# Optimization experiments

Measured on AMD Instinct MI355X. Metric: run time of the kernel, lower is better.

The kernel has to match this reference:

```python
import jax, jax.numpy as jnp
import numpy as np

N, E, C = 100000, 50000, 256
M, D, F, T = 128, 128, 128, 64
MSG = 2 * D + F + T  # 448
T_MAX = 100000


def setup_inputs() -> dict:
    key = jax.random.key(0)
    ks = jax.random.split(key, 16)
    src = jax.random.randint(ks[0], (E,), 0, N, dtype=jnp.int32)
    dst = jax.random.randint(ks[1], (E,), 0, N, dtype=jnp.int32)
    t = jnp.sort(jax.random.randint(ks[2], (E,), 0, T_MAX, dtype=jnp.int32))
    last_update = jax.random.randint(ks[3], (N,), 0, 1000, dtype=jnp.int32)
    event_feat = jax.random.normal(ks[4], (E, F), dtype=jnp.float32)
    src_embeds = jax.random.normal(ks[5], (E, D), dtype=jnp.float32)
    dst_embeds = jax.random.normal(ks[6], (E, D), dtype=jnp.float32)
    nodes_memory = jax.random.normal(ks[7], (N, M), dtype=jnp.float32)
    incidence = jax.random.uniform(ks[8], (N, C), dtype=jnp.float32)
    w_time = jax.random.normal(ks[9], (T,), dtype=jnp.float32)
    b_time = jax.random.normal(ks[10], (T,), dtype=jnp.float32)
    W_ih = jax.random.normal(ks[11], (MSG, 3 * M), dtype=jnp.float32) * 0.05
    W_hh = jax.random.normal(ks[12], (M, 3 * M), dtype=jnp.float32) * 0.05
    b_ih = jnp.zeros((3 * M,), jnp.float32)
    b_hh = jnp.zeros((3 * M,), jnp.float32)
    return dict(src=src, dst=dst, t=t, last_update=last_update,
                event_feat=event_feat, src_embeds=src_embeds, dst_embeds=dst_embeds,
                nodes_memory=nodes_memory, incidence=incidence,
                w_time=w_time, b_time=b_time, W_ih=W_ih, W_hh=W_hh,
                b_ih=b_ih, b_hh=b_hh)


def reference(src, dst, t, last_update, event_feat, src_embeds, dst_embeds,
              nodes_memory, incidence, w_time, b_time, W_ih, W_hh, b_ih, b_hh):
    E2 = 2 * E
    # store_events: raw messages + flipped-direction messages, keyed by source node
    src_all = jnp.concatenate([src, dst])            # [2E]
    emb_s = jnp.concatenate([src_embeds, dst_embeds], axis=0)
    emb_d = jnp.concatenate([dst_embeds, src_embeds], axis=0)
    feat = jnp.concatenate([event_feat, event_feat], axis=0)
    t_all = jnp.concatenate([t, t])                  # [2E]
    # message function: concat(src_embed, dst_embed, event_feat, time_encoding(dt))
    dt = (t_all - last_update[src_all]).astype(jnp.float32)
    time_enc = jnp.cos(dt[:, None] * w_time[None, :] + b_time[None, :])  # [2E, T]
    msg = jnp.concatenate([emb_s, emb_d, feat, time_enc], axis=-1)       # [2E, MSG]
    # 'last' aggregation: per-node argmax over timestamps via rank-encoded segment_max
    perm = jnp.argsort(t_all)  # ascending time order
    rank = jnp.zeros((E2,), jnp.int32).at[perm].set(jnp.arange(E2, dtype=jnp.int32))
    seg_rank = jax.ops.segment_max(rank, src_all, num_segments=N)
    counts = jax.ops.segment_sum(jnp.ones((E2,), jnp.int32), src_all, num_segments=N)
    has_msg = counts > 0                              # [N]
    last_idx = perm[jnp.where(has_msg, seg_rank, 0)]  # [N] event index of last message
    agg_msg = msg[last_idx]                           # [N, MSG]
    # GRU memory updater (torch.nn.GRUCell convention)
    gx = agg_msg @ W_ih + b_ih
    gh = nodes_memory @ W_hh + b_hh
    xr, xz, xn = jnp.split(gx, 3, axis=-1)
    hr, hz, hn = jnp.split(gh, 3, axis=-1)
    r = jax.nn.sigmoid(xr + hr)
    z = jax.nn.sigmoid(xz + hz)
    n = jnp.tanh(xn + r * hn)
    h_new = (1.0 - z) * n + z * nodes_memory
    new_mem = jnp.where(has_msg[:, None], h_new, nodes_memory)  # [N, M]
    # rewire_graph: community memory = incidence.T @ nodes_memory
    comm_mem = jnp.einsum('nc,nm->cm', incidence, new_mem)      # [C, M]
    return jnp.concatenate([new_mem, comm_mem], axis=0)         # [N + C, M]
```

## Files before the change

kernel.cpp:

```cpp
#include <hip/hip_runtime.h>
#include <hip/hip_bf16.h>
#include <stdint.h>

#define N_NODES   100000
#define N_EVENTS  50000
#define N_COMM    256
#define DIM_M     128
#define K_TOT     576
#define GCOLS     512
#define INV2PI    0.15915494309189535f
#define XB_GRID   4096

typedef float f32x4 __attribute__((ext_vector_type(4)));
typedef short s16x8 __attribute__((ext_vector_type(8)));
typedef short s16x4 __attribute__((ext_vector_type(4)));

#define KEYS_OFF   0
#define CNT_OFF    800000
#define LIST_OFF   800008
#define WT_OFF     1200640
#define X_ROWS     100096
#define X_OFF      1790464
#define PART_M_OFF X_OFF
#define CT_NCH     256
#define CT_CPN     392
#define TMP2_OFF   (PART_M_OFF + 33554432)
#define TENC_OFF   1790464
#define PART_F_OFF 14594560

__device__ inline unsigned short f2bf(float x) {
    union { float f; unsigned u; } v; v.f = x;
    unsigned r = v.u + 0x7FFFu + ((v.u >> 16) & 1u);
    return (unsigned short)(r >> 16);
}
__device__ inline float bf2f(unsigned short u) {
    union { unsigned u; float f; } v; v.u = ((unsigned)u) << 16;
    return v.f;
}
__device__ inline float cos_rev(float rev) {
    float fr = rev - floorf(rev);
#if __has_builtin(__builtin_amdgcn_cosf)
    return __builtin_amdgcn_cosf(fr);
#else
    return cosf(fr * 6.283185307179586f);
#endif
}
__device__ inline float sigmoid_f(float x) { return 1.0f / (1.0f + __expf(-x)); }
__device__ inline float tanh_f(float x) {
    float t = __expf(2.0f * x);
    return 1.0f - 2.0f / (t + 1.0f);
}

__global__ __launch_bounds__(256) void k_agg(const int* __restrict__ src,
                                             const int* __restrict__ dst,
                                             const int* __restrict__ t,
                                             unsigned long long* __restrict__ keys) {
    int i = blockIdx.x * 256 + threadIdx.x;
    if (i >= 2 * N_EVENTS) return;
    int e = (i < N_EVENTS) ? i : i - N_EVENTS;
    int node = (i < N_EVENTS) ? src[i] : dst[e];
    unsigned long long key =
        ((unsigned long long)(unsigned)t[e] << 32) | (unsigned)(i + 1);
    atomicMax(&keys[node], key);
}

__global__ __launch_bounds__(256) void k_compact(const unsigned long long* __restrict__ keys,
                                                 unsigned int* __restrict__ cnt,
                                                 int* __restrict__ list) {
    int n = blockIdx.x * 256 + threadIdx.x;
    if (n >= N_NODES) return;
    if (keys[n] != 0ULL) {
        unsigned p = atomicAdd(cnt, 1u);
        list[p] = n;
    }
}

__global__ __launch_bounds__(256) void k_xbuild(
    const unsigned long long* __restrict__ keys,
    const unsigned int* __restrict__ cnt,
    const int* __restrict__ list,
    const int* __restrict__ t,
    const int* __restrict__ last_update,
    const float* __restrict__ event_feat,
    const float* __restrict__ src_embeds,
    const float* __restrict__ dst_embeds,
    const float* __restrict__ mem,
    const float* __restrict__ w_time,
    const float* __restrict__ b_time,
    const float* __restrict__ W_ih,
    const float* __restrict__ W_hh,
    unsigned short* __restrict__ Wt,
    unsigned short* __restrict__ X) {
    if (blockIdx.x >= XB_GRID) {
        int idx = (blockIdx.x - XB_GRID) * 256 + threadIdx.x;
        if (idx >= GCOLS * K_TOT) return;
        int col2 = idx / K_TOT, k = idx % K_TOT;
        int mh = col2 >> 8, rem = col2 & 255;
        int g = rem >> 6, m = mh * 64 + (rem & 63);
        float v;
        if (g == 0)      v = (k < 448) ? W_ih[(size_t)k * 384 + m]
                                       : W_hh[(size_t)(k - 448) * 384 + m];
        else if (g == 1) v = (k < 448) ? W_ih[(size_t)k * 384 + 128 + m]
                                       : W_hh[(size_t)(k - 448) * 384 + 128 + m];
        else if (g == 2) v = (k < 448) ? W_ih[(size_t)k * 384 + 256 + m] : 0.0f;
        else             v = (k < 448) ? 0.0f : W_hh[(size_t)(k - 448) * 384 + 256 + m];
        Wt[idx] = f2bf(v);
        return;
    }
    const unsigned c = *cnt;
    const unsigned cpad = (c + 127u) & ~127u;
    const unsigned total = cpad * 72u;
    for (unsigned idx = blockIdx.x * 256 + threadIdx.x; idx < total;
         idx += XB_GRID * 256) {
        const unsigned row = idx / 72u;
        const int s = (int)(idx - row * 72u);
        unsigned short* xp = X + (size_t)row * K_TOT + s * 8;
        s16x8 v;
        if (row >= c) {
#pragma unroll
            for (int j = 0; j < 8; ++j) v[j] = 0;
            *(s16x8*)xp = v;
            continue;
        }
        const int node = list[row];
        const unsigned long long key = keys[node];
        const int ia = (int)(key & 0xffffffffull) - 1;
        const int e = (ia < N_EVENTS) ? ia : ia - N_EVENTS;
        if (s < 48) {
            const float* p;
            if (s < 16)
                p = ((ia < N_EVENTS) ? src_embeds : dst_embeds) + (size_t)e * 128 + s * 8;
            else if (s < 32)
                p = ((ia < N_EVENTS) ? dst_embeds : src_embeds) + (size_t)e * 128 + (s - 16) * 8;
            else
                p = event_feat + (size_t)e * 128 + (s - 32) * 8;
            float4 a = *(const float4*)p;
            float4 b = *(const float4*)(p + 4);
            v[0] = (short)f2bf(a.x); v[1] = (short)f2bf(a.y);
            v[2] = (short)f2bf(a.z); v[3] = (short)f2bf(a.w);
            v[4] = (short)f2bf(b.x); v[5] = (short)f2bf(b.y);
            v[6] = (short)f2bf(b.z); v[7] = (short)f2bf(b.w);
        } else if (s < 56) {
            const float dt = (float)(t[e] - last_update[node]);
            const int c0 = (s - 48) * 8;
#pragma unroll
            for (int j = 0; j < 8; ++j) {
                float rev = fmaf(dt, w_time[c0 + j] * INV2PI, b_time[c0 + j] * INV2PI);
                v[j] = (short)f2bf(cos_rev(rev));
            }
        } else {
            const float* p = mem + (size_t)node * 128 + (s - 56) * 8;
            float4 a = *(const float4*)p;
            float4 b = *(const float4*)(p + 4);
            v[0] = (short)f2bf(a.x); v[1] = (short)f2bf(a.y);
            v[2] = (short)f2bf(a.z); v[3] = (short)f2bf(a.w);
            v[4] = (short)f2bf(b.x); v[5] = (short)f2bf(b.y);
            v[6] = (short)f2bf(b.z); v[7] = (short)f2bf(b.w);
        }
        *(s16x8*)xp = v;
    }
}

__global__ __launch_bounds__(512, 4) void k_gemm2(
    const unsigned int* __restrict__ cnt,
    const int* __restrict__ list,
    const unsigned short* __restrict__ X,
    const unsigned short* __restrict__ Wt,
    const float* __restrict__ b_ih,
    const float* __restrict__ b_hh,
    float* __restrict__ out) {
    __shared__ unsigned short As[3][128][32];
    __shared__ unsigned short Bs[3][256][32];
    __shared__ int Ls[128];

    const unsigned c = *cnt;
    const int rb = blockIdx.x >> 1;
    const int mh = blockIdx.x & 1;
    const int base = rb * 128;
    if ((unsigned)base >= c) return;
    const int tid = threadIdx.x;
    const int w = tid >> 6, l = tid & 63;
    const int lr = l & 15, lk = l >> 4;
    const int wm = w >> 2, wn = w & 3;

    if (tid < 128)
        Ls[tid] = ((unsigned)(base + tid) < c) ? list[base + tid] : 0;

    const int mcol = mh * 64 + wn * 16 + lr;

    unsigned short hreg[16];
#pragma unroll
    for (int rt = 0; rt < 4; ++rt)
#pragma unroll
        for (int reg = 0; reg < 4; ++reg) {
            const int r = wm * 64 + rt * 16 + lk * 4 + reg;
            hreg[rt * 4 + reg] = X[(size_t)(base + r) * K_TOT + 448 + mcol];
        }

    const int srow = tid >> 2;
    const int sd = tid & 3;
    const int ssl = (sd ^ ((srow >> 1) & 3)) << 3;
    const unsigned short* gA  = X  + (size_t)(base + srow) * K_TOT + ssl;
    const unsigned short* gB0 = Wt + (size_t)(mh * 256 + srow) * K_TOT + ssl;
    const unsigned short* gB1 = Wt + (size_t)(mh * 256 + 128 + srow) * K_TOT + ssl;

#define GLD(SRC, DST) __builtin_amdgcn_global_load_lds( \
        (const __attribute__((address_space(1))) unsigned int*)(SRC), \
        (__attribute__((address_space(3))) unsigned int*)(DST), 16, 0, 0)

    auto stage = [&](int ch, int buf) {
        GLD(gA  + ch * 32, &As[buf][w * 16][0]);
        GLD(gB0 + ch * 32, &Bs[buf][w * 16][0]);
        GLD(gB1 + ch * 32, &Bs[buf][128 + w * 16][0]);
    };

    f32x4 acc[4][4];
#pragma unroll
    for (int rt = 0; rt < 4; ++rt)
#pragma unroll
        for (int i = 0; i < 4; ++i) acc[rt][i] = (f32x4){0.f, 0.f, 0.f, 0.f};

    stage(0, 0);
    stage(1, 1);
    __syncthreads();

#pragma unroll
    for (int ch = 0; ch < 18; ++ch) {
        const int buf = ch % 3;
        if (ch <= 15) stage(ch + 2, (ch + 2) % 3);
        __builtin_amdgcn_s_setprio(1);
        s16x8 a[4];
#pragma unroll
        for (int rt = 0; rt < 4; ++rt) {
            const int r = wm * 64 + rt * 16 + lr;
            const int sl = lk ^ ((r >> 1) & 3);
            a[rt] = *(const s16x8*)&As[buf][r][sl << 3];
        }
#pragma unroll
        for (int i = 0; i < 4; ++i) {
            const int cl = i * 64 + wn * 16 + lr;
            const int slb = lk ^ ((cl >> 1) & 3);
            s16x8 b = *(const s16x8*)&Bs[buf][cl][slb << 3];
#pragma unroll
            for (int rt = 0; rt < 4; ++rt)
                acc[rt][i] = __builtin_amdgcn_mfma_f32_16x16x32_bf16(
                    a[rt], b, acc[rt][i], 0, 0, 0);
        }
        __builtin_amdgcn_s_setprio(0);
        if (ch < 17) {
            __builtin_amdgcn_sched_barrier(0);
            if (ch < 16) asm volatile("s_waitcnt vmcnt(3)" ::: "memory");
            else         asm volatile("s_waitcnt vmcnt(0)" ::: "memory");
            __builtin_amdgcn_s_barrier();
            __builtin_amdgcn_sched_barrier(0);
        }
    }

    const float b_r  = b_ih[mcol] + b_hh[mcol];
    const float b_z  = b_ih[128 + mcol] + b_hh[128 + mcol];
    const float b_xn = b_ih[256 + mcol];
    const float b_hn = b_hh[256 + mcol];
#pragma unroll
    for (int rt = 0; rt < 4; ++rt) {
#pragma unroll
        for (int reg = 0; reg < 4; ++reg) {
            const int r = wm * 64 + rt * 16 + lk * 4 + reg;
            const int grow = base + r;
            if ((unsigned)grow < c) {
                const int node = Ls[r];
                const float h = bf2f(hreg[rt * 4 + reg]);
                float rr = sigmoid_f(acc[rt][0][reg] + b_r);
                float zz = sigmoid_f(acc[rt][1][reg] + b_z);
                float nn = tanh_f(acc[rt][2][reg] + b_xn + rr * (acc[rt][3][reg] + b_hn));
                out[(size_t)node * 128 + mcol] = (1.0f - zz) * nn + zz * h;
            }
        }
    }
#undef GLD
}

__global__ __launch_bounds__(256) void k_copy(const unsigned long long* __restrict__ keys,
                                              const float* __restrict__ nm,
                                              float* __restrict__ out) {
    int idx = blockIdx.x * 256 + threadIdx.x;
    int n = idx >> 5;
    if (n >= N_NODES) return;
    if (keys[n] != 0ULL) return;
    ((float4*)out)[idx] = ((const float4*)nm)[idx];
}

__global__ __launch_bounds__(512) void k_comm_t(const float* __restrict__ inc,
                                                const float* __restrict__ nm,
                                                float* __restrict__ partials) {
    __shared__ unsigned short T[2][12288];

    const int bid = blockIdx.x;
    const int n0 = bid * CT_CPN;
    const int n1 = min(N_NODES, n0 + CT_CPN);
    const int ng = (n1 - n0 + 31) >> 5;
    const int tid = threadIdx.x;
    const int w = tid >> 6, l = tid & 63;
    const int lr = l & 15, lk = l >> 4;

    float vi[4][4];
    float vm[4][2];

    auto load_chunk = [&](int g) {
        const int nb = n0 + g * 32 + w * 4;
#pragma unroll
        for (int ri = 0; ri < 4; ++ri) {
            const int n = nb + ri;
            const bool ok = n < n1;
#pragma unroll
            for (int j = 0; j < 4; ++j)
                vi[ri][j] = ok ? inc[(size_t)n * N_COMM + l + 64 * j] : 0.0f;
#pragma unroll
            for (int j = 0; j < 2; ++j)
                vm[ri][j] = ok ? nm[(size_t)n * DIM_M + l + 64 * j] : 0.0f;
        }
    };
    auto write_chunk = [&](int buf) {
        unsigned short* bi = &T[buf][0];
#pragma unroll
        for (int j = 0; j < 4; ++j) {
            const int cc = l + 64 * j;
            ushort4 p = make_ushort4(f2bf(vi[0][j]), f2bf(vi[1][j]),
                                     f2bf(vi[2][j]), f2bf(vi[3][j]));
            *(ushort4*)&bi[cc * 32 + ((w ^ (cc & 7)) << 2)] = p;
        }
        unsigned short* bm = &T[buf][8192];
#pragma unroll
        for (int j = 0; j < 2; ++j) {
            const int mm = l + 64 * j;
            ushort4 p = make_ushort4(f2bf(vm[0][j]), f2bf(vm[1][j]),
                                     f2bf(vm[2][j]), f2bf(vm[3][j]));
            *(ushort4*)&bm[mm * 32 + ((w ^ (mm & 7)) << 2)] = p;
        }
    };

    f32x4 acc[2][8];
#pragma unroll
    for (int ct = 0; ct < 2; ++ct)
#pragma unroll
        for (int mt = 0; mt < 8; ++mt) acc[ct][mt] = (f32x4){0.f, 0.f, 0.f, 0.f};

    auto compute_chunk = [&](int buf) {
        const unsigned short* bi = &T[buf][0];
        const unsigned short* bm = &T[buf][8192];
        s16x8 a[2];
#pragma unroll
        for (int ct = 0; ct < 2; ++ct) {
            const int cc = (w * 2 + ct) * 16 + lr;
            s16x4 lo = *(const s16x4*)&bi[cc * 32 + (((lk * 2) ^ (cc & 7)) << 2)];
            s16x4 hi = *(const s16x4*)&bi[cc * 32 + (((lk * 2 + 1) ^ (cc & 7)) << 2)];
            a[ct] = __builtin_shufflevector(lo, hi, 0, 1, 2, 3, 4, 5, 6, 7);
        }
#pragma unroll
        for (int mt = 0; mt < 8; ++mt) {
            const int mm = mt * 16 + lr;
            s16x4 lo = *(const s16x4*)&bm[mm * 32 + (((lk * 2) ^ (mm & 7)) << 2)];
            s16x4 hi = *(const s16x4*)&bm[mm * 32 + (((lk * 2 + 1) ^ (mm & 7)) << 2)];
            s16x8 b = __builtin_shufflevector(lo, hi, 0, 1, 2, 3, 4, 5, 6, 7);
            acc[0][mt] = __builtin_amdgcn_mfma_f32_16x16x32_bf16(a[0], b, acc[0][mt], 0, 0, 0);
            acc[1][mt] = __builtin_amdgcn_mfma_f32_16x16x32_bf16(a[1], b, acc[1][mt], 0, 0, 0);
        }
    };

    load_chunk(0);
    write_chunk(0);
    __syncthreads();
    for (int g = 0; g < ng; ++g) {
        if (g + 1 < ng) load_chunk(g + 1);
        compute_chunk(g & 1);
        if (g + 1 < ng) write_chunk((g + 1) & 1);
        __syncthreads();
    }

    float* p = partials + (size_t)bid * (N_COMM * DIM_M);
#pragma unroll
    for (int ct = 0; ct < 2; ++ct) {
#pragma unroll
        for (int mt = 0; mt < 8; ++mt) {
#pragma unroll
            for (int reg = 0; reg < 4; ++reg) {
                const int cc = (w * 2 + ct) * 16 + lk * 4 + reg;
                p[(size_t)cc * DIM_M + mt * 16 + lr] = acc[ct][mt][reg];
            }
        }
    }
}

__global__ __launch_bounds__(256) void k_comm2a(const float* __restrict__ partials,
                                                float* __restrict__ tmp) {
    const int bid = blockIdx.x;
    const int y = bid >> 5, x = bid & 31;
    const int idx4 = x * 256 + threadIdx.x;
    float4 s = make_float4(0.f, 0.f, 0.f, 0.f);
    for (int ci = 0; ci < CT_NCH / 16; ++ci) {
        float4 v = *(const float4*)&partials[(size_t)(y * (CT_NCH / 16) + ci) * (N_COMM * DIM_M) + idx4 * 4];
        s.x += v.x; s.y += v.y; s.z += v.z; s.w += v.w;
    }
    *(float4*)&tmp[(size_t)y * (N_COMM * DIM_M) + idx4 * 4] = s;
}

__global__ __launch_bounds__(256) void k_comm2b(const float* __restrict__ tmp,
                                                float* __restrict__ out) {
    const int idx4 = blockIdx.x * 256 + threadIdx.x;
    float4 s = make_float4(0.f, 0.f, 0.f, 0.f);
    for (int y = 0; y < 16; ++y) {
        float4 v = *(const float4*)&tmp[(size_t)y * (N_COMM * DIM_M) + idx4 * 4];
        s.x += v.x; s.y += v.y; s.z += v.z; s.w += v.w;
    }
    *(float4*)&out[(size_t)N_NODES * DIM_M + idx4 * 4] = s;
}

__global__ __launch_bounds__(256) void k_wconv_old(const float* __restrict__ W_ih,
                                                   const float* __restrict__ W_hh,
                                                   unsigned short* __restrict__ Wt) {
    int idx = blockIdx.x * 256 + threadIdx.x;
    if (idx >= GCOLS * K_TOT) return;
    int col = idx / K_TOT, k = idx % K_TOT;
    float v;
    if (col < 256) {
        v = (k < 448) ? W_ih[(size_t)k * 384 + col]
                      : W_hh[(size_t)(k - 448) * 384 + col];
    } else if (col < 384) {
        v = (k < 448) ? W_ih[(size_t)k * 384 + col] : 0.0f;
    } else {
        v = (k < 448) ? 0.0f : W_hh[(size_t)(k - 448) * 384 + (col - 128)];
    }
    Wt[idx] = f2bf(v);
}

__global__ __launch_bounds__(256) void k_tenc(const unsigned long long* __restrict__ keys,
                                              const unsigned int* __restrict__ cnt,
                                              const int* __restrict__ list,
                                              const int* __restrict__ t,
                                              const int* __restrict__ last_update,
                                              const float* __restrict__ w_time,
                                              const float* __restrict__ b_time,
                                              unsigned short* __restrict__ tenc) {
    int idx = blockIdx.x * 256 + threadIdx.x;
    int r = idx >> 3, slot = idx & 7;
    const unsigned c = *cnt;
    const unsigned cpad = (c + 63u) & ~63u;
    if ((unsigned)r >= cpad) return;
    s16x8 v;
    if ((unsigned)r < c) {
        int node = list[r];
        unsigned long long key = keys[node];
        int ia = (int)(key & 0xffffffffull) - 1;
        int e = (ia < N_EVENTS) ? ia : ia - N_EVENTS;
        float dt = (float)(t[e] - last_update[node]);
#pragma unroll
        for (int j = 0; j < 8; ++j) {
            int cix = slot * 8 + j;
            float arg = __fadd_rn(__fmul_rn(dt, w_time[cix]), b_time[cix]);
            v[j] = (short)f2bf(cosf(arg));
        }
    } else {
#pragma unroll
        for (int j = 0; j < 8; ++j) v[j] = 0;
    }
    *(s16x8*)&tenc[(size_t)r * 64 + slot * 8] = v;
}

__global__ __launch_bounds__(256, 2) void k_gemm_fused(
    const unsigned long long* __restrict__ keys,
    const unsigned int* __restrict__ cnt,
    const int* __restrict__ list,
    const float* __restrict__ event_feat,
    const float* __restrict__ src_embeds,
    const float* __restrict__ dst_embeds,
    const float* __restrict__ mem,
    const unsigned short* __restrict__ tenc,
    const unsigned short* __restrict__ Wt,
    const float* __restrict__ b_ih,
    const float* __restrict__ b_hh,
    float* __restrict__ out) {
    __shared__ unsigned short Xs[2][4][64][8];

    const unsigned c = *cnt;
    const int base = blockIdx.x * 64;
    if ((unsigned)base >= c) return;
    const int tid = threadIdx.x;

    const int srow = tid >> 2;
    const int kslot = tid & 3;
    const int sgrow = base + srow;
    const bool valid = (unsigned)sgrow < c;
    const float *p_es = nullptr, *p_ed = nullptr, *p_ef = nullptr, *p_mem = nullptr;
    const unsigned short* p_te = nullptr;
    if (valid) {
        int node = list[sgrow];
        unsigned long long key = keys[node];
        int ia = (int)(key & 0xffffffffull) - 1;
        int e = (ia < N_EVENTS) ? ia : ia - N_EVENTS;
        const float* sp = src_embeds + (size_t)e * 128;
        const float* dp = dst_embeds + (size_t)e * 128;
        p_es = (ia < N_EVENTS) ? sp : dp;
        p_ed = (ia < N_EVENTS) ? dp : sp;
        p_ef = event_feat + (size_t)e * 128;
        p_te = tenc + (size_t)sgrow * 64;
        p_mem = mem + (size_t)node * 128;
    }

    auto stage = [&](int ch) {
        const int buf = ch & 1;
        const int k0 = ch * 32 + kslot * 8;
        s16x8 v;
        if (valid) {
            if (k0 < 384) {
                const float* p = (k0 < 128) ? (p_es + k0)
                               : (k0 < 256) ? (p_ed + (k0 - 128))
                                            : (p_ef + (k0 - 256));
                float4 a = *(const float4*)p;
                float4 b = *(const float4*)(p + 4);
                v[0] = (short)f2bf(a.x); v[1] = (short)f2bf(a.y);
                v[2] = (short)f2bf(a.z); v[3] = (short)f2bf(a.w);
                v[4] = (short)f2bf(b.x); v[5] = (short)f2bf(b.y);
                v[6] = (short)f2bf(b.z); v[7] = (short)f2bf(b.w);
            } else if (k0 < 448) {
                v = *(const s16x8*)(p_te + (k0 - 384));
            } else {
                const float* p = p_mem + (k0 - 448);
                float4 a = *(const float4*)p;
                float4 b = *(const float4*)(p + 4);
                v[0] = (short)f2bf(a.x); v[1] = (short)f2bf(a.y);
                v[2] = (short)f2bf(a.z); v[3] = (short)f2bf(a.w);
                v[4] = (short)f2bf(b.x); v[5] = (short)f2bf(b.y);
                v[6] = (short)f2bf(b.z); v[7] = (short)f2bf(b.w);
            }
        } else {
#pragma unroll
            for (int j = 0; j < 8; ++j) v[j] = 0;
        }
        *(s16x8*)&Xs[buf][kslot][srow][0] = v;
    };

    const int w = tid >> 6;
    const int l = tid & 63;
    const int lr = l & 15;
    const int lk = l >> 4;

    f32x4 acc[4][8];
#pragma unroll
    for (int rt = 0; rt < 4; ++rt)
#pragma unroll
        for (int i = 0; i < 8; ++i) acc[rt][i] = (f32x4){0.f, 0.f, 0.f, 0.f};

    stage(0);
    __syncthreads();

    for (int ch = 0; ch < 18; ++ch) {
        if (ch < 17) stage(ch + 1);
        const int buf = ch & 1;
        s16x8 a[4];
#pragma unroll
        for (int rt = 0; rt < 4; ++rt)
            a[rt] = *(const s16x8*)&Xs[buf][lk][rt * 16 + lr][0];
#pragma unroll
        for (int i = 0; i < 8; ++i) {
            const int col = (w + 4 * i) * 16 + lr;
            s16x8 b = *(const s16x8*)&Wt[(size_t)col * K_TOT + ch * 32 + lk * 8];
#pragma unroll
            for (int rt = 0; rt < 4; ++rt)
                acc[rt][i] = __builtin_amdgcn_mfma_f32_16x16x32_bf16(
                    a[rt], b, acc[rt][i], 0, 0, 0);
        }
        __syncthreads();
    }

#pragma unroll
    for (int jj = 0; jj < 2; ++jj) {
        const int mcol = (w + 4 * jj) * 16 + lr;
        const float b_r  = b_ih[mcol] + b_hh[mcol];
        const float b_z  = b_ih[128 + mcol] + b_hh[128 + mcol];
        const float b_xn = b_ih[256 + mcol];
        const float b_hn = b_hh[256 + mcol];
#pragma unroll
        for (int rt = 0; rt < 4; ++rt) {
#pragma unroll
            for (int reg = 0; reg < 4; ++reg) {
                const int grow = base + rt * 16 + lk * 4 + reg;
                if ((unsigned)grow < c) {
                    const int node = list[grow];
                    const float h = mem[(size_t)node * 128 + mcol];
                    float rr = sigmoid_f(acc[rt][0 + jj][reg] + b_r);
                    float zz = sigmoid_f(acc[rt][2 + jj][reg] + b_z);
                    float nn = tanh_f(acc[rt][4 + jj][reg] + b_xn +
                                      rr * (acc[rt][6 + jj][reg] + b_hn));
                    out[(size_t)node * 128 + mcol] = (1.0f - zz) * nn + zz * h;
                }
            }
        }
    }
}

__global__ __launch_bounds__(256) void k_comm1(const float* __restrict__ inc,
                                               const float* __restrict__ nm,
                                               float* __restrict__ partials,
                                               int nch, int cpn) {
    __shared__ float inc_s[2][8][128];
    __shared__ float mem_s[2][8][128];

    const int bid = blockIdx.x;
    const int ct2 = bid / nch;
    const int ch  = bid % nch;
    const int n0 = ch * cpn;
    const int n1 = min(N_NODES, n0 + cpn);
    const int tid = threadIdx.x;

    const int srow = tid >> 5;
    const int scol = (tid & 31) * 4;

    auto stage = [&](int g, int buf) {
        const int n = n0 + g * 8 + srow;
        float4 iv = make_float4(0.f, 0.f, 0.f, 0.f);
        float4 mv = make_float4(0.f, 0.f, 0.f, 0.f);
        if (n < n1) {
            iv = *(const float4*)(inc + (size_t)n * N_COMM + ct2 * 128 + scol);
            mv = *(const float4*)(nm + (size_t)n * DIM_M + scol);
        }
        *(float4*)&inc_s[buf][srow][scol] = iv;
        *(float4*)&mem_s[buf][srow][scol] = mv;
    };

    const int c0 = (tid >> 3) * 4;
    const int mb = (tid & 7) * 4;

    float acc[4][4][4];
#pragma unroll
    for (int a = 0; a < 4; ++a)
#pragma unroll
        for (int b = 0; b < 4; ++b)
#pragma unroll
            for (int d = 0; d < 4; ++d) acc[a][b][d] = 0.0f;

    const int ngrp = (n1 - n0 + 7) >> 3;
    stage(0, 0);
    __syncthreads();

    for (int g = 0; g < ngrp; ++g) {
        if (g + 1 < ngrp) stage(g + 1, (g + 1) & 1);
        const int buf = g & 1;
#pragma unroll
        for (int i = 0; i < 8; ++i) {
            const float4 cv = *(const float4*)&inc_s[buf][i][c0];
            const float ca[4] = {cv.x, cv.y, cv.z, cv.w};
#pragma unroll
            for (int j = 0; j < 4; ++j) {
                const float4 mv = *(const float4*)&mem_s[buf][i][j * 32 + mb];
                const float ma[4] = {mv.x, mv.y, mv.z, mv.w};
#pragma unroll
                for (int ci = 0; ci < 4; ++ci)
#pragma unroll
                    for (int mi = 0; mi < 4; ++mi)
                        acc[ci][j][mi] = fmaf(ca[ci], ma[mi], acc[ci][j][mi]);
            }
        }
        __syncthreads();
    }

    float* p = partials + (size_t)bid * (128 * 128);
#pragma unroll
    for (int ci = 0; ci < 4; ++ci)
#pragma unroll
        for (int j = 0; j < 4; ++j)
            *(float4*)(p + (size_t)(c0 + ci) * 128 + j * 32 + mb) =
                make_float4(acc[ci][j][0], acc[ci][j][1], acc[ci][j][2], acc[ci][j][3]);
}

__global__ __launch_bounds__(256) void k_comm2_f(const float* __restrict__ partials,
                                                 float* __restrict__ out,
                                                 int nch) {
    int idx = blockIdx.x * 256 + threadIdx.x;
    if (idx >= N_COMM * DIM_M) return;
    int cg = idx >> 7;
    int m = idx & 127;
    int ct2 = cg >> 7;
    int cl = cg & 127;
    float s = 0.0f;
    for (int ch = 0; ch < nch; ++ch)
        s += partials[((size_t)ct2 * nch + ch) * 16384 + (size_t)cl * 128 + m];
    out[(size_t)N_NODES * DIM_M + idx] = s;
}

extern "C" void kernel_launch(void* const* d_in, const int* in_sizes, int n_in,
                              void* d_out, int out_size, void* d_ws, size_t ws_size,
                              hipStream_t stream) {
    const int* src          = (const int*)d_in[0];
    const int* dst          = (const int*)d_in[1];
    const int* t            = (const int*)d_in[2];
    const int* last_update  = (const int*)d_in[3];
    const float* event_feat = (const float*)d_in[4];
    const float* src_embeds = (const float*)d_in[5];
    const float* dst_embeds = (const float*)d_in[6];
    const float* nodes_mem  = (const float*)d_in[7];
    const float* incidence  = (const float*)d_in[8];
    const float* w_time     = (const float*)d_in[9];
    const float* b_time     = (const float*)d_in[10];
    const float* W_ih       = (const float*)d_in[11];
    const float* W_hh       = (const float*)d_in[12];
    const float* b_ih       = (const float*)d_in[13];
    const float* b_hh       = (const float*)d_in[14];
    float* out = (float*)d_out;

    char* ws = (char*)d_ws;
    unsigned long long* keys = (unsigned long long*)(ws + KEYS_OFF);
    unsigned int* cnt        = (unsigned int*)(ws + CNT_OFF);
    int* list                = (int*)(ws + LIST_OFF);
    unsigned short* Wt       = (unsigned short*)(ws + WT_OFF);

    const bool xfit = ws_size >= (size_t)X_OFF + (size_t)X_ROWS * (K_TOT * 2);

    hipMemsetAsync(d_ws, 0, LIST_OFF, stream);

    k_agg<<<(2 * N_EVENTS + 255) / 256, 256, 0, stream>>>(src, dst, t, keys);
    k_compact<<<(N_NODES + 255) / 256, 256, 0, stream>>>(keys, cnt, list);

    if (xfit) {
        unsigned short* X = (unsigned short*)(ws + X_OFF);
        float* partials   = (float*)(ws + PART_M_OFF);
        float* tmp2       = (float*)(ws + TMP2_OFF);

        const int wconv_blocks = (GCOLS * K_TOT + 255) / 256;
        k_xbuild<<<XB_GRID + wconv_blocks, 256, 0, stream>>>(
            keys, cnt, list, t, last_update, event_feat, src_embeds, dst_embeds,
            nodes_mem, w_time, b_time, W_ih, W_hh, Wt, X);
        k_gemm2<<<(X_ROWS / 128) * 2, 512, 0, stream>>>(cnt, list, X, Wt, b_ih, b_hh, out);
        k_copy<<<(N_NODES * 32 + 255) / 256, 256, 0, stream>>>(keys, nodes_mem, out);
        k_comm_t<<<CT_NCH, 512, 0, stream>>>(incidence, out, partials);
        k_comm2a<<<512, 256, 0, stream>>>(partials, tmp2);
        k_comm2b<<<32, 256, 0, stream>>>(tmp2, out);
    } else {
        unsigned short* tenc = (unsigned short*)(ws + TENC_OFF);
        float* partials      = (float*)(ws + PART_F_OFF);
        int NCH = 512;
        while (NCH > 8 && (size_t)PART_F_OFF + (size_t)NCH * 131072 > ws_size) NCH >>= 1;
        int cpn = (N_NODES + NCH - 1) / NCH;

        k_wconv_old<<<(GCOLS * K_TOT + 255) / 256, 256, 0, stream>>>(W_ih, W_hh, Wt);
        k_tenc<<<(100032 * 8) / 256, 256, 0, stream>>>(keys, cnt, list, t, last_update,
                                                       w_time, b_time, tenc);
        k_gemm_fused<<<100032 / 64, 256, 0, stream>>>(keys, cnt, list, event_feat,
                                                      src_embeds, dst_embeds, nodes_mem,
                                                      tenc, Wt, b_ih, b_hh, out);
        k_copy<<<(N_NODES * 32 + 255) / 256, 256, 0, stream>>>(keys, nodes_mem, out);
        k_comm1<<<2 * NCH, 256, 0, stream>>>(incidence, out, partials, NCH, cpn);
        k_comm2_f<<<(N_COMM * DIM_M + 255) / 256, 256, 0, stream>>>(partials, out, NCH);
    }
}
```

Baseline: 201.8 us.

## Fuse memory copy into GEMM launch, double comm split, vectorize partial stores

Adds extra blocks to the GEMM kernel that copy untouched node memory rows, removing the separate copy launch. Doubles the number of chunks in the community reduction (shorter per-block node range) and adjusts the two reduction stages accordingly. Partial results are now stored as contiguous float4 in MFMA register order, with the final reduction remapping to the output layout. This trades more partial-sum traffic (twice the partial buffer) for more parallelism and coalesced writes.

New measurement: 221.0 us. 9.5% more time.

```diff
diff --git a/kernel.cpp b/kernel.cpp
--- a/kernel.cpp
+++ b/kernel.cpp
@@ -22,9 +22,9 @@
 #define X_ROWS     100096
 #define X_OFF      1790464
 #define PART_M_OFF X_OFF
-#define CT_NCH     256
-#define CT_CPN     392
-#define TMP2_OFF   (PART_M_OFF + 33554432)
+#define CT_NCH     512
+#define CT_CPN     196
+#define TMP2_OFF   (PART_M_OFF + 67108864)
 #define TENC_OFF   1790464
 #define PART_F_OFF 14594560
 
@@ -161,17 +161,31 @@
     }
 }
 
+#define NGEMM ((X_ROWS / 128) * 2)
+#define NCOPY 256
 __global__ __launch_bounds__(512, 4) void k_gemm2(
+    const unsigned long long* __restrict__ keys,
     const unsigned int* __restrict__ cnt,
     const int* __restrict__ list,
     const unsigned short* __restrict__ X,
     const unsigned short* __restrict__ Wt,
+    const float* __restrict__ nmem,
     const float* __restrict__ b_ih,
     const float* __restrict__ b_hh,
     float* __restrict__ out) {
     __shared__ unsigned short As[3][128][32];
     __shared__ unsigned short Bs[3][256][32];
     __shared__ int Ls[128];
+
+    if (blockIdx.x >= NGEMM) {
+        const int b = blockIdx.x - NGEMM;
+        for (int idx = b * 512 + threadIdx.x; idx < N_NODES * 32; idx += NCOPY * 512) {
+            const int n = idx >> 5;
+            if (keys[n] == 0ULL)
+                ((float4*)out)[idx] = ((const float4*)nmem)[idx];
+        }
+        return;
+    }
 
     const unsigned c = *cnt;
     const int rb = blockIdx.x >> 1;
@@ -378,16 +392,10 @@
 
     float* p = partials + (size_t)bid * (N_COMM * DIM_M);
 #pragma unroll
-    for (int ct = 0; ct < 2; ++ct) {
-#pragma unroll
-        for (int mt = 0; mt < 8; ++mt) {
-#pragma unroll
-            for (int reg = 0; reg < 4; ++reg) {
-                const int cc = (w * 2 + ct) * 16 + lk * 4 + reg;
-                p[(size_t)cc * DIM_M + mt * 16 + lr] = acc[ct][mt][reg];
-            }
-        }
-    }
+    for (int ct = 0; ct < 2; ++ct)
+#pragma unroll
+        for (int mt = 0; mt < 8; ++mt)
+            *(f32x4*)&p[(size_t)(((ct * 8 + mt) * 512) + tid) * 4] = acc[ct][mt];
 }
 
 __global__ __launch_bounds__(256) void k_comm2a(const float* __restrict__ partials,
@@ -396,8 +404,8 @@
     const int y = bid >> 5, x = bid & 31;
     const int idx4 = x * 256 + threadIdx.x;
     float4 s = make_float4(0.f, 0.f, 0.f, 0.f);
-    for (int ci = 0; ci < CT_NCH / 16; ++ci) {
-        float4 v = *(const float4*)&partials[(size_t)(y * (CT_NCH / 16) + ci) * (N_COMM * DIM_M) + idx4 * 4];
+    for (int ci = 0; ci < CT_NCH / 32; ++ci) {
+        float4 v = *(const float4*)&partials[(size_t)(y * (CT_NCH / 32) + ci) * (N_COMM * DIM_M) + idx4 * 4];
         s.x += v.x; s.y += v.y; s.z += v.z; s.w += v.w;
     }
     *(float4*)&tmp[(size_t)y * (N_COMM * DIM_M) + idx4 * 4] = s;
@@ -407,11 +415,22 @@
                                                 float* __restrict__ out) {
     const int idx4 = blockIdx.x * 256 + threadIdx.x;
     float4 s = make_float4(0.f, 0.f, 0.f, 0.f);
-    for (int y = 0; y < 16; ++y) {
+    for (int y = 0; y < 32; ++y) {
         float4 v = *(const float4*)&tmp[(size_t)y * (N_COMM * DIM_M) + idx4 * 4];
         s.x += v.x; s.y += v.y; s.z += v.z; s.w += v.w;
     }
-    *(float4*)&out[(size_t)N_NODES * DIM_M + idx4 * 4] = s;
+    const int q = idx4 >> 9;
+    const int tid = idx4 & 511;
+    const int ct = q >> 3, mt = q & 7;
+    const int w = tid >> 6, l = tid & 63;
+    const int lr = l & 15, lk = l >> 4;
+    const int mm = mt * 16 + lr;
+    const float sv[4] = {s.x, s.y, s.z, s.w};
+#pragma unroll
+    for (int reg = 0; reg < 4; ++reg) {
+        const int cc = (w * 2 + ct) * 16 + lk * 4 + reg;
+        out[(size_t)N_NODES * DIM_M + (size_t)cc * DIM_M + mm] = sv[reg];
+    }
 }
 
 __global__ __launch_bounds__(256) void k_wconv_old(const float* __restrict__ W_ih,
@@ -728,10 +747,10 @@
         k_xbuild<<<XB_GRID + wconv_blocks, 256, 0, stream>>>(
             keys, cnt, list, t, last_update, event_feat, src_embeds, dst_embeds,
             nodes_mem, w_time, b_time, W_ih, W_hh, Wt, X);
-        k_gemm2<<<(X_ROWS / 128) * 2, 512, 0, stream>>>(cnt, list, X, Wt, b_ih, b_hh, out);
-        k_copy<<<(N_NODES * 32 + 255) / 256, 256, 0, stream>>>(keys, nodes_mem, out);
+        k_gemm2<<<NGEMM + NCOPY, 512, 0, stream>>>(keys, cnt, list, X, Wt,
+                                                   nodes_mem, b_ih, b_hh, out);
         k_comm_t<<<CT_NCH, 512, 0, stream>>>(incidence, out, partials);
-        k_comm2a<<<512, 256, 0, stream>>>(partials, tmp2);
+        k_comm2a<<<1024, 256, 0, stream>>>(partials, tmp2);
         k_comm2b<<<32, 256, 0, stream>>>(tmp2, out);
     } else {
         unsigned short* tenc = (unsigned short*)(ws + TENC_OFF);
```
